# Optimization experiments

Hardware: AMD Instinct MI355X
Metric: run time of the kernel (lower is better)

Reference implementation:

```python
import jax, jax.numpy as jnp
import numpy as np

N_NODES = 100000
N_EDGES = 1600000
D_IN = 128
D_OUT = 128
NUM_NEIGHBORS = 10


def setup_inputs() -> dict:
    key = jax.random.key(0)
    k1, k2, k3, k4 = jax.random.split(key, 4)
    x = jax.random.normal(k1, (N_NODES, D_IN), dtype=jnp.float32)
    edge_index = jax.random.randint(k2, (2, N_EDGES), 0, N_NODES, dtype=jnp.int64)
    W = jax.random.normal(k3, (D_OUT, D_IN), dtype=jnp.float32) / np.sqrt(D_IN)
    b = jax.random.normal(k4, (D_OUT,), dtype=jnp.float32) * 0.01
    return {"x": x, "edge_index": edge_index, "W": W, "b": b}


def reference(x, edge_index, W, b):
    # Torch semantics: for each node, take the FIRST num_neighbors edges
    # (in original edge order) with row==node, mean their col features;
    # fall back to x[node] if the node has no out-edges. Then linear.
    row, col = edge_index[0], edge_index[1]
    N, E = x.shape[0], row.shape[0]
    # Stable sort by row preserves within-row edge order, so "first k per row"
    # is identical to the torch masking loop.
    order = jnp.argsort(row, stable=True)
    row_s = row[order]
    col_s = col[order]
    # Index of first edge of each row segment -> per-edge rank within segment.
    starts = jnp.searchsorted(row_s, jnp.arange(N, dtype=row_s.dtype))
    rank = jnp.arange(E) - starts[row_s]
    keep = (rank < NUM_NEIGHBORS).astype(x.dtype)  # [E]
    # Masked gather + segment sum == sampled neighbor mean numerator.
    feats = x[col_s] * keep[:, None]               # [E, D_IN] (gather-bound)
    sums = jax.ops.segment_sum(feats, row_s, num_segments=N)
    counts = jax.ops.segment_sum(keep, row_s, num_segments=N)  # [N]
    agg = jnp.where(counts[:, None] > 0,
                    sums / jnp.maximum(counts, 1.0)[:, None],
                    x)
    return agg @ W.T + b
```

## Files before the change

### kernel.cpp

```cpp
#include <hip/hip_runtime.h>
#include <hip/hip_bf16.h>
#include <cstdint>
#include <cstddef>

#define D 128
#define KNB 10
#define SENT 0x7FFFFFFF
#define SHIFT 8
#define NPB 256
#define T_BIN 256
#define EPB 4096
#define MAXNB 1024

typedef __attribute__((ext_vector_type(8))) short short8;
typedef __attribute__((ext_vector_type(4))) float floatx4;

__device__ inline unsigned bf16_rne(float f) {
  unsigned u = __builtin_bit_cast(unsigned, f);
  return (u + 0x7FFFu + ((u >> 16) & 1u)) >> 16;
}

__global__ __launch_bounds__(256) void k_init2(int* __restrict__ counts, int NB,
                                               int* __restrict__ slots, int S) {
  int i = blockIdx.x * 256 + threadIdx.x;
  if (i < NB) counts[i] = 0;
  if (i < S) slots[i] = SENT;
}

__global__ __launch_bounds__(T_BIN) void k_count_xcast(const int* __restrict__ row, int E,
                                                       int NB, int* __restrict__ counts,
                                                       int blocks_bin,
                                                       const float* __restrict__ x,
                                                       unsigned* __restrict__ xh, int n8) {
  if ((int)blockIdx.x < blocks_bin) {
    __shared__ int hist[MAXNB];
    for (int i = threadIdx.x; i < NB; i += T_BIN) hist[i] = 0;
    __syncthreads();
    int e0 = blockIdx.x * EPB;
    for (int i = threadIdx.x; i < EPB; i += T_BIN) {
      int e = e0 + i;
      if (e < E) atomicAdd(&hist[row[e] >> SHIFT], 1);
    }
    __syncthreads();
    for (int i = threadIdx.x; i < NB; i += T_BIN)
      if (hist[i]) atomicAdd(&counts[i], hist[i]);
  } else {
    int t = ((int)blockIdx.x - blocks_bin) * T_BIN + threadIdx.x;
    if (t >= n8) return;
    const float4* p = reinterpret_cast<const float4*>(x) + (size_t)t * 2;
    float4 a = p[0], b = p[1];
    uint4 o;
    o.x = bf16_rne(a.x) | (bf16_rne(a.y) << 16);
    o.y = bf16_rne(a.z) | (bf16_rne(a.w) << 16);
    o.z = bf16_rne(b.x) | (bf16_rne(b.y) << 16);
    o.w = bf16_rne(b.z) | (bf16_rne(b.w) << 16);
    reinterpret_cast<uint4*>(xh)[t] = o;
  }
}

__global__ __launch_bounds__(MAXNB) void k_scan(const int* __restrict__ counts, int NB,
                                                int* __restrict__ bases,
                                                int* __restrict__ cursor) {
  __shared__ int buf[MAXNB];
  int t = threadIdx.x;
  int v = (t < NB) ? counts[t] : 0;
  buf[t] = v;
  __syncthreads();
  for (int off = 1; off < MAXNB; off <<= 1) {
    int xv = (t >= off) ? buf[t - off] : 0;
    __syncthreads();
    buf[t] += xv;
    __syncthreads();
  }
  if (t < NB) {
    int base = buf[t] - v;
    bases[t] = base;
    cursor[t] = base;
  }
}

__global__ __launch_bounds__(T_BIN) void k_scatter2(const int* __restrict__ row, int E,
                                                    int NB, int* __restrict__ cursor,
                                                    unsigned* __restrict__ binned) {
  __shared__ int hist[MAXNB];
  __shared__ int lbase[MAXNB];
  for (int i = threadIdx.x; i < NB; i += T_BIN) hist[i] = 0;
  __syncthreads();
  int e0 = blockIdx.x * EPB;
  for (int i = threadIdx.x; i < EPB; i += T_BIN) {
    int e = e0 + i;
    if (e < E) atomicAdd(&hist[row[e] >> SHIFT], 1);
  }
  __syncthreads();
  for (int i = threadIdx.x; i < NB; i += T_BIN) {
    int h = hist[i];
    lbase[i] = h ? atomicAdd(&cursor[i], h) : 0;
  }
  __syncthreads();
  for (int i = threadIdx.x; i < NB; i += T_BIN) hist[i] = 0;
  __syncthreads();
  for (int i = threadIdx.x; i < EPB; i += T_BIN) {
    int e = e0 + i;
    if (e < E) {
      int r = row[e];
      int b = r >> SHIFT;
      int pos = lbase[b] + atomicAdd(&hist[b], 1);
      binned[pos] = ((unsigned)(r & (NPB - 1)) << 24) | (unsigned)e;
    }
  }
}

__global__ __launch_bounds__(256) void k_select(const unsigned* __restrict__ binned,
                                                const int* __restrict__ bases,
                                                const int* __restrict__ counts,
                                                int* __restrict__ slots_g, int N, int E) {
  __shared__ int sl[NPB * KNB];
  int b = blockIdx.x;
  int nbase = b << SHIFT;
  int nloc = min(NPB, N - nbase);
  for (int i = threadIdx.x; i < nloc * KNB; i += 256) sl[i] = SENT;
  __syncthreads();
  int base = bases[b];
  int cnt = counts[b];
  if (cnt > E) cnt = E;
  for (int i = threadIdx.x; i < cnt; i += 256) {
    unsigned en = binned[base + i];
    int rl = (int)(en >> 24);
    int v = (int)(en & 0xFFFFFFu);
    int* s = &sl[rl * KNB];
#pragma unroll
    for (int k = 0; k < KNB; ++k) {
      int old = atomicMin(&s[k], v);
      if (old == SENT) break;
      v = v > old ? v : old;
    }
  }
  __syncthreads();
  for (int i = threadIdx.x; i < nloc * KNB; i += 256)
    slots_g[(size_t)nbase * KNB + i] = sl[i];
}

__global__ __launch_bounds__(256) void k_agg_hb(const unsigned* __restrict__ xh,
                                                const float* __restrict__ x,
                                                const int* __restrict__ ei,
                                                const int* __restrict__ slots,
                                                unsigned* __restrict__ aggbh,
                                                int N, int E) {
  int wave = threadIdx.x >> 6;
  int lane = threadIdx.x & 63;
  int n = blockIdx.x * 4 + wave;
  if (n >= N) return;

  int eid = SENT;
  if (lane < KNB) eid = slots[(size_t)n * KNB + lane];
  bool valid = (lane < KNB) && ((unsigned)eid < (unsigned)E);
  int nsel = __popcll(__ballot(valid));
  int c = valid ? ei[(size_t)E + eid] : -1;

  unsigned uu[KNB];
  float wj[KNB];
#pragma unroll
  for (int j = 0; j < KNB; ++j) {
    int cj = __shfl(c, j);
    bool vj = (unsigned)cj < (unsigned)N;
    wj[j] = vj ? 1.f : 0.f;
    uu[j] = xh[(size_t)(vj ? cj : 0) * 64 + lane];
  }

  float ax = 0.f, ay = 0.f;
  if (nsel > 0) {
#pragma unroll
    for (int j = 0; j < KNB; ++j) {
      ax += wj[j] * __builtin_bit_cast(float, uu[j] << 16);
      ay += wj[j] * __builtin_bit_cast(float, uu[j] & 0xFFFF0000u);
    }
    float sc = 1.f / (float)nsel;
    ax *= sc; ay *= sc;
  } else {
    float2 v = reinterpret_cast<const float2*>(x + (size_t)n * D)[lane];
    ax = v.x; ay = v.y;
  }
  aggbh[(size_t)n * 64 + lane] = bf16_rne(ax) | (bf16_rne(ay) << 16);
}

__global__ __launch_bounds__(256) void k_agg_h(const unsigned* __restrict__ xh,
                                               const float* __restrict__ x,
                                               const int* __restrict__ ei,
                                               const int* __restrict__ slots,
                                               float* __restrict__ agg, int N, int E) {
  int wave = threadIdx.x >> 6;
  int lane = threadIdx.x & 63;
  int n = blockIdx.x * 4 + wave;
  if (n >= N) return;
  int eid = SENT;
  if (lane < KNB) eid = slots[(size_t)n * KNB + lane];
  bool valid = (lane < KNB) && ((unsigned)eid < (unsigned)E);
  unsigned long long m = __ballot(valid);
  int nsel = __popcll(m);
  int c = valid ? ei[(size_t)E + eid] : 0;
  float ax = 0.f, ay = 0.f;
  if (nsel > 0) {
    unsigned long long mm = m;
    while (mm) {
      int j = (int)__builtin_ctzll(mm);
      mm &= mm - 1;
      int cj = __shfl(c, j);
      if ((unsigned)cj >= (unsigned)N) cj = 0;
      unsigned u = xh[(size_t)cj * 64 + lane];
      ax += __builtin_bit_cast(float, u << 16);
      ay += __builtin_bit_cast(float, u & 0xFFFF0000u);
    }
    float sc = 1.f / (float)nsel;
    ax *= sc; ay *= sc;
  } else {
    float2 v = reinterpret_cast<const float2*>(x + (size_t)n * D)[lane];
    ax = v.x; ay = v.y;
  }
  reinterpret_cast<float2*>(agg + (size_t)n * D)[lane] = make_float2(ax, ay);
}

__global__ __launch_bounds__(256) void k_agg(const float* __restrict__ x,
                                             const int* __restrict__ ei,
                                             const int* __restrict__ slots,
                                             float* __restrict__ agg,
                                             int N, int E) {
  int wave = threadIdx.x >> 6;
  int lane = threadIdx.x & 63;
  int n = blockIdx.x * 4 + wave;
  if (n >= N) return;
  int eid = SENT;
  if (lane < KNB) eid = slots[(size_t)n * KNB + lane];
  bool valid = (lane < KNB) && ((unsigned)eid < (unsigned)E);
  unsigned long long m = __ballot(valid);
  int nsel = __popcll(m);
  int c = valid ? ei[(size_t)E + eid] : 0;
  float2 acc = make_float2(0.f, 0.f);
  if (nsel > 0) {
    unsigned long long mm = m;
    while (mm) {
      int j = (int)__builtin_ctzll(mm);
      mm &= mm - 1;
      int cj = __shfl(c, j);
      if ((unsigned)cj >= (unsigned)N) cj = 0;
      float2 v = reinterpret_cast<const float2*>(x + (size_t)cj * D)[lane];
      acc.x += v.x; acc.y += v.y;
    }
    float sc = 1.f / (float)nsel;
    acc.x *= sc; acc.y *= sc;
  } else {
    acc = reinterpret_cast<const float2*>(x + (size_t)n * D)[lane];
  }
  reinterpret_cast<float2*>(agg + (size_t)n * D)[lane] = acc;
}

#define GBN 128
#define LDK 136

__global__ __launch_bounds__(256) void k_gemm_bf(const unsigned short* __restrict__ aggbh,
                                                 const float* __restrict__ Wm,
                                                 const float* __restrict__ bias,
                                                 float* __restrict__ out, int N) {
  __shared__ unsigned short sA[GBN * LDK];
  __shared__ unsigned short sW[GBN * LDK];
  const int tid = threadIdx.x;
  const int n0 = blockIdx.x * GBN;

#pragma unroll
  for (int i = 0; i < 8; ++i) {
    int q = i * 256 + tid;
    int row = q >> 4;
    int c16 = q & 15;
    uint4 v = make_uint4(0u, 0u, 0u, 0u);
    if (n0 + row < N)
      v = reinterpret_cast<const uint4*>(aggbh + (size_t)(n0 + row) * D)[c16];
    *reinterpret_cast<uint4*>(&sA[row * LDK + c16 * 8]) = v;
  }
#pragma unroll
  for (int i = 0; i < 16; ++i) {
    int q = i * 256 + tid;
    int row = q >> 5;
    int c4 = q & 31;
    float4 wv = reinterpret_cast<const float4*>(Wm + (size_t)row * D)[c4];
    ushort4 uw;
    uw.x = (unsigned short)bf16_rne(wv.x);
    uw.y = (unsigned short)bf16_rne(wv.y);
    uw.z = (unsigned short)bf16_rne(wv.z);
    uw.w = (unsigned short)bf16_rne(wv.w);
    *reinterpret_cast<ushort4*>(&sW[row * LDK + c4 * 4]) = uw;
  }
  __syncthreads();

  const int wave = tid >> 6;
  const int lane = tid & 63;
  const int lrow = lane & 15;
  const int quad = lane >> 4;

  floatx4 acc[2][8];
#pragma unroll
  for (int mt = 0; mt < 2; ++mt)
#pragma unroll
    for (int nt = 0; nt < 8; ++nt)
      acc[mt][nt] = (floatx4){0.f, 0.f, 0.f, 0.f};

  float bv[8];
#pragma unroll
  for (int nt = 0; nt < 8; ++nt) bv[nt] = bias[nt * 16 + lrow];

#pragma unroll
  for (int ks = 0; ks < 4; ++ks) {
    int koff = ks * 32 + quad * 8;
    short8 a0 = *reinterpret_cast<const short8*>(&sA[(wave * 32 + lrow) * LDK + koff]);
    short8 a1 = *reinterpret_cast<const short8*>(&sA[(wave * 32 + 16 + lrow) * LDK + koff]);
#pragma unroll
    for (int nt = 0; nt < 8; ++nt) {
      short8 b = *reinterpret_cast<const short8*>(&sW[(nt * 16 + lrow) * LDK + koff]);
      acc[0][nt] = __builtin_amdgcn_mfma_f32_16x16x32_bf16(a0, b, acc[0][nt], 0, 0, 0);
      acc[1][nt] = __builtin_amdgcn_mfma_f32_16x16x32_bf16(a1, b, acc[1][nt], 0, 0, 0);
    }
  }

#pragma unroll
  for (int mt = 0; mt < 2; ++mt) {
    int rbase = n0 + wave * 32 + mt * 16 + quad * 4;
#pragma unroll
    for (int reg = 0; reg < 4; ++reg) {
      int r = rbase + reg;
      if (r < N) {
        float* op = out + (size_t)r * D + lrow;
#pragma unroll
        for (int nt = 0; nt < 8; ++nt)
          op[nt * 16] = acc[mt][nt][reg] + bv[nt];
      }
    }
  }
}

#define BN 128
#define KC 32
#define LDP 132

__global__ __launch_bounds__(256) void k_gemm(const float* __restrict__ agg,
                                              const float* __restrict__ Wm,
                                              const float* __restrict__ bias,
                                              float* __restrict__ out, int N) {
  __shared__ float sA[KC][LDP];
  __shared__ float sW[KC][LDP];
  const int tid = threadIdx.x;
  const int tx = tid & 15;
  const int ty = tid >> 4;
  const int n0 = blockIdx.x * BN;

  float acc[8][8];
#pragma unroll
  for (int i = 0; i < 8; ++i)
#pragma unroll
    for (int j = 0; j < 8; ++j) acc[i][j] = 0.f;

  const int nl = tid >> 3;
  const int kq = tid & 7;

  for (int kc = 0; kc < D; kc += KC) {
#pragma unroll
    for (int i = 0; i < 4; ++i) {
      int rrow = nl + i * 32;
      int n = n0 + rrow;
      float4 av = make_float4(0.f, 0.f, 0.f, 0.f);
      if (n < N)
        av = reinterpret_cast<const float4*>(agg + (size_t)n * D + kc)[kq];
      int k = kq * 4;
      sA[k+0][rrow] = av.x; sA[k+1][rrow] = av.y;
      sA[k+2][rrow] = av.z; sA[k+3][rrow] = av.w;
      float4 wv = reinterpret_cast<const float4*>(Wm + (size_t)rrow * D + kc)[kq];
      sW[k+0][rrow] = wv.x; sW[k+1][rrow] = wv.y;
      sW[k+2][rrow] = wv.z; sW[k+3][rrow] = wv.w;
    }
    __syncthreads();
#pragma unroll
    for (int k = 0; k < KC; ++k) {
      float4 a0 = *reinterpret_cast<const float4*>(&sA[k][ty * 8]);
      float4 a1 = *reinterpret_cast<const float4*>(&sA[k][ty * 8 + 4]);
      float4 w0 = *reinterpret_cast<const float4*>(&sW[k][tx * 8]);
      float4 w1 = *reinterpret_cast<const float4*>(&sW[k][tx * 8 + 4]);
      float a[8] = {a0.x, a0.y, a0.z, a0.w, a1.x, a1.y, a1.z, a1.w};
      float w[8] = {w0.x, w0.y, w0.z, w0.w, w1.x, w1.y, w1.z, w1.w};
#pragma unroll
      for (int i = 0; i < 8; ++i)
#pragma unroll
        for (int j = 0; j < 8; ++j)
          acc[i][j] += a[i] * w[j];
    }
    __syncthreads();
  }

  float4 b0 = reinterpret_cast<const float4*>(bias)[tx * 2];
  float4 b1 = reinterpret_cast<const float4*>(bias)[tx * 2 + 1];
#pragma unroll
  for (int i = 0; i < 8; ++i) {
    int n = n0 + ty * 8 + i;
    if (n < N) {
      float4 v0 = make_float4(acc[i][0] + b0.x, acc[i][1] + b0.y,
                              acc[i][2] + b0.z, acc[i][3] + b0.w);
      float4 v1 = make_float4(acc[i][4] + b1.x, acc[i][5] + b1.y,
                              acc[i][6] + b1.z, acc[i][7] + b1.w);
      float4* op = reinterpret_cast<float4*>(out + (size_t)n * D + tx * 8);
      op[0] = v0;
      op[1] = v1;
    }
  }
}

extern "C" void kernel_launch(void* const* d_in, const int* in_sizes, int n_in,
                              void* d_out, int out_size, void* d_ws, size_t ws_size,
                              hipStream_t stream) {
  const float* x    = (const float*)d_in[0];
  const int*   ei   = (const int*)d_in[1];
  const float* Wm   = (const float*)d_in[2];
  const float* bias = (const float*)d_in[3];
  float* out = (float*)d_out;

  const int N = in_sizes[0] / D;
  const int E = in_sizes[1] / 2;
  const int NB = (N + NPB - 1) >> SHIFT;

  int* counts = (int*)d_ws;
  int* bases  = counts + NB;
  int* cursor = bases + NB;
  size_t off_slots = ((size_t)(3 * NB) * 4 + 15) & ~(size_t)15;
  int* slots = (int*)((char*)d_ws + off_slots);
  size_t off_xh = (off_slots + (size_t)N * KNB * 4 + 15) & ~(size_t)15;
  unsigned* xh = (unsigned*)((char*)d_ws + off_xh);
  size_t off_ab = off_xh + (size_t)N * D * 2;
  unsigned* aggbh = (unsigned*)((char*)d_ws + off_ab);

  const bool have_xh = ws_size >= off_xh + (size_t)N * D * 2;
  const bool have_ab = ws_size >= off_ab + (size_t)N * D * 2;

  unsigned* binned = (unsigned*)d_out;
  const int blocks_bin = (E + EPB - 1) / EPB;
  const int S = N * KNB;
  const int n8 = N * (D / 8);
  const int xblocks = have_xh ? (n8 + T_BIN - 1) / T_BIN : 0;

  k_init2<<<(S + 255) / 256, 256, 0, stream>>>(counts, NB, slots, S);
  k_count_xcast<<<blocks_bin + xblocks, T_BIN, 0, stream>>>(ei, E, NB, counts,
                                                            blocks_bin, x, xh, n8);
  k_scan<<<1, MAXNB, 0, stream>>>(counts, NB, bases, cursor);
  k_scatter2<<<blocks_bin, T_BIN, 0, stream>>>(ei, E, NB, cursor, binned);
  k_select<<<NB, 256, 0, stream>>>(binned, bases, counts, slots, N, E);

  if (have_ab) {
    k_agg_hb<<<(N + 3) / 4, 256, 0, stream>>>(xh, x, ei, slots, aggbh, N, E);
    k_gemm_bf<<<(N + GBN - 1) / GBN, 256, 0, stream>>>(
        (const unsigned short*)aggbh, Wm, bias, out, N);
  } else if (have_xh) {
    k_agg_h<<<(N + 3) / 4, 256, 0, stream>>>(xh, x, ei, slots, out, N, E);
    k_gemm<<<(N + BN - 1) / BN, 256, 0, stream>>>(out, Wm, bias, out, N);
  } else {
    k_agg<<<(N + 3) / 4, 256, 0, stream>>>(x, ei, slots, out, N, E);
    k_gemm<<<(N + BN - 1) / BN, 256, 0, stream>>>(out, Wm, bias, out, N);
  }
}
```

Measured before the change: 239.4 us.

## Resolve neighbor columns in select, drop slot init, pack 4 nodes per wave in aggregation

Result: faster. 232.5 us (-2.9%).

```diff
diff --git a/kernel.cpp b/kernel.cpp
--- a/kernel.cpp
+++ b/kernel.cpp
@@ -19,12 +19,12 @@
   unsigned u = __builtin_bit_cast(unsigned, f);
   return (u + 0x7FFFu + ((u >> 16) & 1u)) >> 16;
 }
-
-__global__ __launch_bounds__(256) void k_init2(int* __restrict__ counts, int NB,
-                                               int* __restrict__ slots, int S) {
+__device__ inline float bflo(unsigned u) { return __builtin_bit_cast(float, u << 16); }
+__device__ inline float bfhi(unsigned u) { return __builtin_bit_cast(float, u & 0xFFFF0000u); }
+
+__global__ __launch_bounds__(256) void k_init(int* __restrict__ counts, int NB) {
   int i = blockIdx.x * 256 + threadIdx.x;
   if (i < NB) counts[i] = 0;
-  if (i < S) slots[i] = SENT;
 }
 
 __global__ __launch_bounds__(T_BIN) void k_count_xcast(const int* __restrict__ row, int E,
@@ -113,6 +113,7 @@
 __global__ __launch_bounds__(256) void k_select(const unsigned* __restrict__ binned,
                                                 const int* __restrict__ bases,
                                                 const int* __restrict__ counts,
+                                                const int* __restrict__ ei,
                                                 int* __restrict__ slots_g, int N, int E) {
   __shared__ int sl[NPB * KNB];
   int b = blockIdx.x;
@@ -136,68 +137,90 @@
     }
   }
   __syncthreads();
-  for (int i = threadIdx.x; i < nloc * KNB; i += 256)
-    slots_g[(size_t)nbase * KNB + i] = sl[i];
+  for (int i = threadIdx.x; i < nloc * KNB; i += 256) {
+    int v = sl[i];
+    int col = ((unsigned)v < (unsigned)E) ? ei[(size_t)E + v] : -1;
+    slots_g[(size_t)nbase * KNB + i] = col;
+  }
 }
 
 __global__ __launch_bounds__(256) void k_agg_hb(const unsigned* __restrict__ xh,
                                                 const float* __restrict__ x,
-                                                const int* __restrict__ ei,
                                                 const int* __restrict__ slots,
                                                 unsigned* __restrict__ aggbh,
-                                                int N, int E) {
+                                                int N) {
+  const int lane = threadIdx.x & 63;
+  const int j16 = lane & 15;
+  const int gsh = lane & 48;
+  const int n = blockIdx.x * 16 + (threadIdx.x >> 4);
+  const bool active = n < N;
+
+  int scol = -1;
+  if (active && j16 < KNB) scol = slots[(size_t)n * KNB + j16];
+  bool valid = (unsigned)scol < (unsigned)N;
+  unsigned long long bal = __ballot(valid);
+  int nsel = __popc((unsigned)((bal >> gsh) & 0xFFFFull));
+
+  int ck[KNB];
+#pragma unroll
+  for (int k = 0; k < KNB; ++k) ck[k] = __shfl(scol, gsh + k);
+
+  const uint4* xh4 = reinterpret_cast<const uint4*>(xh);
+  uint4 uu[KNB];
+  float wj[KNB];
+#pragma unroll
+  for (int k = 0; k < KNB; ++k) {
+    bool vk = (unsigned)ck[k] < (unsigned)N;
+    wj[k] = vk ? 1.f : 0.f;
+    uu[k] = xh4[(size_t)(vk ? ck[k] : 0) * 16 + j16];
+  }
+
+  if (!active) return;
+
+  float acc[8];
+#pragma unroll
+  for (int q = 0; q < 8; ++q) acc[q] = 0.f;
+
+  if (nsel > 0) {
+#pragma unroll
+    for (int k = 0; k < KNB; ++k) {
+      float w = wj[k];
+      acc[0] += w * bflo(uu[k].x); acc[1] += w * bfhi(uu[k].x);
+      acc[2] += w * bflo(uu[k].y); acc[3] += w * bfhi(uu[k].y);
+      acc[4] += w * bflo(uu[k].z); acc[5] += w * bfhi(uu[k].z);
+      acc[6] += w * bflo(uu[k].w); acc[7] += w * bfhi(uu[k].w);
+    }
+    float sc = 1.f / (float)nsel;
+#pragma unroll
+    for (int q = 0; q < 8; ++q) acc[q] *= sc;
+  } else {
+    const float4* xr = reinterpret_cast<const float4*>(x + (size_t)n * D);
+    float4 v0 = xr[j16 * 2], v1 = xr[j16 * 2 + 1];
+    acc[0] = v0.x; acc[1] = v0.y; acc[2] = v0.z; acc[3] = v0.w;
+    acc[4] = v1.x; acc[5] = v1.y; acc[6] = v1.z; acc[7] = v1.w;
+  }
+
+  uint4 o;
+  o.x = bf16_rne(acc[0]) | (bf16_rne(acc[1]) << 16);
+  o.y = bf16_rne(acc[2]) | (bf16_rne(acc[3]) << 16);
+  o.z = bf16_rne(acc[4]) | (bf16_rne(acc[5]) << 16);
+  o.w = bf16_rne(acc[6]) | (bf16_rne(acc[7]) << 16);
+  reinterpret_cast<uint4*>(aggbh)[(size_t)n * 16 + j16] = o;
+}
+
+__global__ __launch_bounds__(256) void k_agg_h(const unsigned* __restrict__ xh,
+                                               const float* __restrict__ x,
+                                               const int* __restrict__ slots,
+                                               float* __restrict__ agg, int N) {
   int wave = threadIdx.x >> 6;
   int lane = threadIdx.x & 63;
   int n = blockIdx.x * 4 + wave;
   if (n >= N) return;
-
-  int eid = SENT;
-  if (lane < KNB) eid = slots[(size_t)n * KNB + lane];
-  bool valid = (lane < KNB) && ((unsigned)eid < (unsigned)E);
-  int nsel = __popcll(__ballot(valid));
-  int c = valid ? ei[(size_t)E + eid] : -1;
-
-  unsigned uu[KNB];
-  float wj[KNB];
-#pragma unroll
-  for (int j = 0; j < KNB; ++j) {
-    int cj = __shfl(c, j);
-    bool vj = (unsigned)cj < (unsigned)N;
-    wj[j] = vj ? 1.f : 0.f;
-    uu[j] = xh[(size_t)(vj ? cj : 0) * 64 + lane];
-  }
-
-  float ax = 0.f, ay = 0.f;
-  if (nsel > 0) {
-#pragma unroll
-    for (int j = 0; j < KNB; ++j) {
-      ax += wj[j] * __builtin_bit_cast(float, uu[j] << 16);
-      ay += wj[j] * __builtin_bit_cast(float, uu[j] & 0xFFFF0000u);
-    }
-    float sc = 1.f / (float)nsel;
-    ax *= sc; ay *= sc;
-  } else {
-    float2 v = reinterpret_cast<const float2*>(x + (size_t)n * D)[lane];
-    ax = v.x; ay = v.y;
-  }
-  aggbh[(size_t)n * 64 + lane] = bf16_rne(ax) | (bf16_rne(ay) << 16);
-}
-
-__global__ __launch_bounds__(256) void k_agg_h(const unsigned* __restrict__ xh,
-                                               const float* __restrict__ x,
-                                               const int* __restrict__ ei,
-                                               const int* __restrict__ slots,
-                                               float* __restrict__ agg, int N, int E) {
-  int wave = threadIdx.x >> 6;
-  int lane = threadIdx.x & 63;
-  int n = blockIdx.x * 4 + wave;
-  if (n >= N) return;
-  int eid = SENT;
-  if (lane < KNB) eid = slots[(size_t)n * KNB + lane];
-  bool valid = (lane < KNB) && ((unsigned)eid < (unsigned)E);
+  int c = -1;
+  if (lane < KNB) c = slots[(size_t)n * KNB + lane];
+  bool valid = (lane < KNB) && ((unsigned)c < (unsigned)N);
   unsigned long long m = __ballot(valid);
   int nsel = __popcll(m);
-  int c = valid ? ei[(size_t)E + eid] : 0;
   float ax = 0.f, ay = 0.f;
   if (nsel > 0) {
     unsigned long long mm = m;
@@ -207,8 +230,8 @@
       int cj = __shfl(c, j);
       if ((unsigned)cj >= (unsigned)N) cj = 0;
       unsigned u = xh[(size_t)cj * 64 + lane];
-      ax += __builtin_bit_cast(float, u << 16);
-      ay += __builtin_bit_cast(float, u & 0xFFFF0000u);
+      ax += bflo(u);
+      ay += bfhi(u);
     }
     float sc = 1.f / (float)nsel;
     ax *= sc; ay *= sc;
@@ -220,20 +243,18 @@
 }
 
 __global__ __launch_bounds__(256) void k_agg(const float* __restrict__ x,
-                                             const int* __restrict__ ei,
                                              const int* __restrict__ slots,
                                              float* __restrict__ agg,
-                                             int N, int E) {
+                                             int N) {
   int wave = threadIdx.x >> 6;
   int lane = threadIdx.x & 63;
   int n = blockIdx.x * 4 + wave;
   if (n >= N) return;
-  int eid = SENT;
-  if (lane < KNB) eid = slots[(size_t)n * KNB + lane];
-  bool valid = (lane < KNB) && ((unsigned)eid < (unsigned)E);
+  int c = -1;
+  if (lane < KNB) c = slots[(size_t)n * KNB + lane];
+  bool valid = (lane < KNB) && ((unsigned)c < (unsigned)N);
   unsigned long long m = __ballot(valid);
   int nsel = __popcll(m);
-  int c = valid ? ei[(size_t)E + eid] : 0;
   float2 acc = make_float2(0.f, 0.f);
   if (nsel > 0) {
     unsigned long long mm = m;
@@ -437,26 +458,25 @@
 
   unsigned* binned = (unsigned*)d_out;
   const int blocks_bin = (E + EPB - 1) / EPB;
-  const int S = N * KNB;
   const int n8 = N * (D / 8);
   const int xblocks = have_xh ? (n8 + T_BIN - 1) / T_BIN : 0;
 
-  k_init2<<<(S + 255) / 256, 256, 0, stream>>>(counts, NB, slots, S);
+  k_init<<<(NB + 255) / 256, 256, 0, stream>>>(counts, NB);
   k_count_xcast<<<blocks_bin + xblocks, T_BIN, 0, stream>>>(ei, E, NB, counts,
                                                             blocks_bin, x, xh, n8);
   k_scan<<<1, MAXNB, 0, stream>>>(counts, NB, bases, cursor);
   k_scatter2<<<blocks_bin, T_BIN, 0, stream>>>(ei, E, NB, cursor, binned);
-  k_select<<<NB, 256, 0, stream>>>(binned, bases, counts, slots, N, E);
+  k_select<<<NB, 256, 0, stream>>>(binned, bases, counts, ei, slots, N, E);
 
   if (have_ab) {
-    k_agg_hb<<<(N + 3) / 4, 256, 0, stream>>>(xh, x, ei, slots, aggbh, N, E);
+    k_agg_hb<<<(N + 15) / 16, 256, 0, stream>>>(xh, x, slots, aggbh, N);
     k_gemm_bf<<<(N + GBN - 1) / GBN, 256, 0, stream>>>(
         (const unsigned short*)aggbh, Wm, bias, out, N);
   } else if (have_xh) {
-    k_agg_h<<<(N + 3) / 4, 256, 0, stream>>>(xh, x, ei, slots, out, N, E);
+    k_agg_h<<<(N + 3) / 4, 256, 0, stream>>>(xh, x, slots, out, N);
     k_gemm<<<(N + BN - 1) / BN, 256, 0, stream>>>(out, Wm, bias, out, N);
   } else {
-    k_agg<<<(N + 3) / 4, 256, 0, stream>>>(x, ei, slots, out, N, E);
+    k_agg<<<(N + 3) / 4, 256, 0, stream>>>(x, slots, out, N);
     k_gemm<<<(N + BN - 1) / BN, 256, 0, stream>>>(out, Wm, bias, out, N);
   }
 }
```
